# Performance work log

Measured on AMD Instinct MI355X. Metric: run time of the kernel, lower is better.

The kernel has to match this reference:

```python
import jax, jax.numpy as jnp
import numpy as np
from math import log2, ceil

NUM_LEAVES = 128
KERNEL = 8
STRIDE = 8
PADDING = 0
LR = 0.3

LEAF_NUM = 2 ** ceil(log2(NUM_LEAVES))   # 128
DEPTH = int(log2(LEAF_NUM))              # 7
NUM_NODES = 2 * LEAF_NUM - 1             # 255


def _ancestor_table():
    # A[j-1, t-1] = global heap index of the ancestor of node j at tree level t,
    # or -1 if t exceeds j's own level. Nodes use heap indexing: children of i
    # are 2i+1, 2i+2 (matches the layer bookkeeping in the torch module).
    A = np.full((NUM_NODES - 1, DEPTH), -1, dtype=np.int32)
    for j in range(1, NUM_NODES):
        lvl = int(np.floor(np.log2(j + 1)))
        anc = j
        for t in range(lvl, 0, -1):
            A[j - 1, t - 1] = anc
            anc = (anc - 1) // 2
    return jnp.asarray(A)

_ANC = _ancestor_table()  # (NUM_NODES-1, DEPTH)


def img2patches(x):
    x = jnp.pad(x, PADDING)
    H, W = x.shape
    n0 = (H - KERNEL) // STRIDE + 1
    n1 = (W - KERNEL) // STRIDE + 1
    win = jnp.arange(KERNEL)
    rows = jnp.arange(n0)[:, None] * STRIDE + win[None, :]  # (n0, k)
    cols = jnp.arange(n1)[:, None] * STRIDE + win[None, :]  # (n1, k)
    p = x[rows[:, None, :, None], cols[None, :, None, :]]   # (n0, n1, k, k)
    return p.reshape(n0 * n1, KERNEL * KERNEL)


def setup_inputs() -> dict:
    key = jax.random.key(0)
    k1, k2 = jax.random.split(key)
    image = jax.random.uniform(k1, (2048, 2048), dtype=jnp.float32)
    nodes = jax.random.uniform(k2, (NUM_NODES, KERNEL * KERNEL), dtype=jnp.float32)
    return {"image": image, "nodes": nodes}


def reference(image, nodes):
    X = img2patches(image)                      # (P, k^2)
    P = X.shape[0]

    # --- hierarchical BMU descent (binary tree, DEPTH levels) ---
    cur = jnp.zeros((P,), dtype=jnp.int32)      # root
    bmu_levels = []
    for _ in range(DEPTH):
        c0 = 2 * cur + 1
        c1 = 2 * cur + 2
        # pnorm with p=2 in the source is (sum((a-b)^2))^2 -- monotone, kept faithful
        d0 = jnp.sum((nodes[c0] - X) ** 2, axis=-1) ** 2
        d1 = jnp.sum((nodes[c1] - X) ** 2, axis=-1) ** 2
        cur = jnp.where(d1 < d0, c1, c0)        # tie -> first (c0), like torch.min
        bmu_levels.append(cur)
    bmu_path = jnp.stack(bmu_levels, axis=1)    # (P, DEPTH), bmu at levels 1..DEPTH

    # --- layer_state for every non-root node: number of levels at which the
    # node's ancestor coincides with the BMU chain (== the torch concatenated
    # layer_state, columns ordered by global node index 1..NUM_NODES-1) ---
    state = jnp.sum(_ANC[None, :, :] == bmu_path[:, None, :], axis=-1)  # (P, N-1)

    lrates = LR * (2.0 ** jnp.arange(1, DEPTH + 2, dtype=jnp.float32)) / 2.0 ** (DEPTH + 1)
    lrs = lrates[state]                          # (P, N-1)

    # mean_p lrs[p,j] * (X[p,:] - nodes[1+j,:])
    #   = (lrs^T @ X)/P - mean_p(lrs)[:,None] * nodes[1:]
    upd = jnp.einsum('pj,pk->jk', lrs, X) / P - lrs.mean(axis=0)[:, None] * nodes[1:]
    new_nodes = nodes.at[1:].add(upd)

    return new_nodes, cur[:, None]               # updated codebook, leaf BMU per patch
```

## Files before the change

### kernel.cpp

```cpp
#include <hip/hip_runtime.h>

#define IMG_W 2048
#define NUM_NODES 255
#define NLEAF 128
#define DEPTH 7
#define RS 68
#define NBLK 256
#define NUPD 16

template<int CTRL>
__device__ __forceinline__ float dpp_add(float x) {
    int v = __builtin_amdgcn_update_dpp(0, __float_as_int(x), CTRL, 0xF, 0xF, true);
    return x + __int_as_float(v);
}
__device__ __forceinline__ float group16_sum(float x) {
    x = dpp_add<0xB1>(x);
    x = dpp_add<0x4E>(x);
    x = dpp_add<0x141>(x);
    x = dpp_add<0x128>(x);
    return x;
}

__global__ __launch_bounds__(1024, 4) void fusedK(const float* __restrict__ img,
                                                  const float* __restrict__ nodes,
                                                  float* __restrict__ leaf_out,
                                                  float* __restrict__ S,
                                                  unsigned* __restrict__ cnt,
                                                  unsigned* __restrict__ fdone,
                                                  float* __restrict__ out_nodes)
{
    __shared__ float nds[NUM_NODES * RS];
    __shared__ float Sl[NLEAF * RS];
    __shared__ unsigned cntl[NLEAF];

    const int t = threadIdx.x;
    const int b = blockIdx.x;
    const int g = t >> 4;
    const int q = t & 15;
    const int q4 = q * 4;

    for (int i = t; i < NLEAF * RS; i += 1024) Sl[i] = 0.0f;
    if (t < NLEAF) cntl[t] = 0u;

    const float4* ng = (const float4*)nodes;
    for (int i = t; i < NUM_NODES * 16; i += 1024) {
        *(float4*)&nds[(i >> 4) * RS + (i & 15) * 4] = ng[i];
    }

    float4 xv0, xv1, xv2, xv3;
    {
        const int roff = (q >> 1), coff = (q & 1) * 4;
        int p = b * 256 + g;
        xv0 = *(const float4*)(img + (size_t)((p >> 8) * 8 + roff) * IMG_W + (p & 255) * 8 + coff);
        p += 64;
        xv1 = *(const float4*)(img + (size_t)((p >> 8) * 8 + roff) * IMG_W + (p & 255) * 8 + coff);
        p += 64;
        xv2 = *(const float4*)(img + (size_t)((p >> 8) * 8 + roff) * IMG_W + (p & 255) * 8 + coff);
        p += 64;
        xv3 = *(const float4*)(img + (size_t)((p >> 8) * 8 + roff) * IMG_W + (p & 255) * 8 + coff);
    }
    __syncthreads();

    int cur0 = 0, cur1 = 0, cur2 = 0, cur3 = 0;
    #pragma unroll
    for (int lvl = 0; lvl < DEPTH; ++lvl) {
        const int ca = 2 * cur0 + 1;
        const int cb = 2 * cur1 + 1;
        const int cc = 2 * cur2 + 1;
        const int cd = 2 * cur3 + 1;
        const float* pa = &nds[ca * RS + q4];
        const float* pb = &nds[cb * RS + q4];
        const float* pc = &nds[cc * RS + q4];
        const float* pd = &nds[cd * RS + q4];
        const float4 A0 = *(const float4*)(pa);
        const float4 B0 = *(const float4*)(pa + RS);
        const float4 A1 = *(const float4*)(pb);
        const float4 B1 = *(const float4*)(pb + RS);
        const float4 A2 = *(const float4*)(pc);
        const float4 B2 = *(const float4*)(pc + RS);
        const float4 A3 = *(const float4*)(pd);
        const float4 B3 = *(const float4*)(pd + RS);

        float d, s0, s1;
        s0 = 0.f; s1 = 0.f;
        d = A0.x - xv0.x; s0 = fmaf(d, d, s0);  d = B0.x - xv0.x; s1 = fmaf(d, d, s1);
        d = A0.y - xv0.y; s0 = fmaf(d, d, s0);  d = B0.y - xv0.y; s1 = fmaf(d, d, s1);
        d = A0.z - xv0.z; s0 = fmaf(d, d, s0);  d = B0.z - xv0.z; s1 = fmaf(d, d, s1);
        d = A0.w - xv0.w; s0 = fmaf(d, d, s0);  d = B0.w - xv0.w; s1 = fmaf(d, d, s1);
        cur0 = (group16_sum(s1 - s0) < 0.0f) ? (ca + 1) : ca;
        s0 = 0.f; s1 = 0.f;
        d = A1.x - xv1.x; s0 = fmaf(d, d, s0);  d = B1.x - xv1.x; s1 = fmaf(d, d, s1);
        d = A1.y - xv1.y; s0 = fmaf(d, d, s0);  d = B1.y - xv1.y; s1 = fmaf(d, d, s1);
        d = A1.z - xv1.z; s0 = fmaf(d, d, s0);  d = B1.z - xv1.z; s1 = fmaf(d, d, s1);
        d = A1.w - xv1.w; s0 = fmaf(d, d, s0);  d = B1.w - xv1.w; s1 = fmaf(d, d, s1);
        cur1 = (group16_sum(s1 - s0) < 0.0f) ? (cb + 1) : cb;
        s0 = 0.f; s1 = 0.f;
        d = A2.x - xv2.x; s0 = fmaf(d, d, s0);  d = B2.x - xv2.x; s1 = fmaf(d, d, s1);
        d = A2.y - xv2.y; s0 = fmaf(d, d, s0);  d = B2.y - xv2.y; s1 = fmaf(d, d, s1);
        d = A2.z - xv2.z; s0 = fmaf(d, d, s0);  d = B2.z - xv2.z; s1 = fmaf(d, d, s1);
        d = A2.w - xv2.w; s0 = fmaf(d, d, s0);  d = B2.w - xv2.w; s1 = fmaf(d, d, s1);
        cur2 = (group16_sum(s1 - s0) < 0.0f) ? (cc + 1) : cc;
        s0 = 0.f; s1 = 0.f;
        d = A3.x - xv3.x; s0 = fmaf(d, d, s0);  d = B3.x - xv3.x; s1 = fmaf(d, d, s1);
        d = A3.y - xv3.y; s0 = fmaf(d, d, s0);  d = B3.y - xv3.y; s1 = fmaf(d, d, s1);
        d = A3.z - xv3.z; s0 = fmaf(d, d, s0);  d = B3.z - xv3.z; s1 = fmaf(d, d, s1);
        d = A3.w - xv3.w; s0 = fmaf(d, d, s0);  d = B3.w - xv3.w; s1 = fmaf(d, d, s1);
        cur3 = (group16_sum(s1 - s0) < 0.0f) ? (cd + 1) : cd;
    }

    if (q == 0) {
        leaf_out[b * 256 + g]       = (float)cur0;
        leaf_out[b * 256 + 64 + g]  = (float)cur1;
        leaf_out[b * 256 + 128 + g] = (float)cur2;
        leaf_out[b * 256 + 192 + g] = (float)cur3;
        atomicAdd(&cntl[cur0 - 127], 1u);
        atomicAdd(&cntl[cur1 - 127], 1u);
        atomicAdd(&cntl[cur2 - 127], 1u);
        atomicAdd(&cntl[cur3 - 127], 1u);
    }

    {
        float* base = &Sl[(cur0 - 127) * RS + q];
        atomicAdd(base +  0, xv0.x); atomicAdd(base + 16, xv0.y);
        atomicAdd(base + 32, xv0.z); atomicAdd(base + 48, xv0.w);
        base = &Sl[(cur1 - 127) * RS + q];
        atomicAdd(base +  0, xv1.x); atomicAdd(base + 16, xv1.y);
        atomicAdd(base + 32, xv1.z); atomicAdd(base + 48, xv1.w);
        base = &Sl[(cur2 - 127) * RS + q];
        atomicAdd(base +  0, xv2.x); atomicAdd(base + 16, xv2.y);
        atomicAdd(base + 32, xv2.z); atomicAdd(base + 48, xv2.w);
        base = &Sl[(cur3 - 127) * RS + q];
        atomicAdd(base +  0, xv3.x); atomicAdd(base + 16, xv3.y);
        atomicAdd(base + 32, xv3.z); atomicAdd(base + 48, xv3.w);
    }
    __syncthreads();

    for (int ii = t; ii < NLEAF * 64; ii += 1024) {
        const int i = (ii + b * 64) & (NLEAF * 64 - 1);
        const int e = i & 63;
        const float v = Sl[(i >> 6) * RS + (e & 3) * 16 + (e >> 2)];
        if (v != 0.0f) atomicAdd(&S[i], v);
    }
    if (t < NLEAF && cntl[t] != 0u) atomicAdd(&cnt[t], cntl[t]);

    __syncthreads();
    if (t == 0) {
        __threadfence();
        __hip_atomic_fetch_add(fdone, 1u, __ATOMIC_RELEASE, __HIP_MEMORY_SCOPE_AGENT);
    }
    if (b >= NUPD) return;

    if (t == 0) {
        while (__hip_atomic_load(fdone, __ATOMIC_ACQUIRE, __HIP_MEMORY_SCOPE_AGENT) != NBLK) {}
    }
    __syncthreads();

    float* Ss = nds;
    float* cs = nds + 8192;
    for (int i = t; i < NLEAF * 64; i += 1024)
        Ss[i] = __hip_atomic_load(&S[i], __ATOMIC_RELAXED, __HIP_MEMORY_SCOPE_AGENT);
    if (t < NLEAF)
        cs[t] = (float)__hip_atomic_load(&cnt[t], __ATOMIC_RELAXED, __HIP_MEMORY_SCOPE_AGENT);
    __syncthreads();

    const int n = b * 16 + (t >> 6);
    const int k = t & 63;
    if (n >= NUM_NODES) return;
    const float nd = nodes[n * 64 + k];
    float o;
    if (n == 0) {
        o = nd;
    } else {
        const int pos = n + 1;
        const int Ln = 31 - __clz(pos);
        float su = 0.f, sc = 0.f;
        #pragma unroll 8
        for (int L = 0; L < NLEAF; ++L) {
            const int a = (128 + L) >> (7 - Ln);
            const int x = pos ^ a;
            const int state = (x == 0) ? Ln : (Ln - (31 - __clz(x)) - 1);
            const float lr = 0.3f * ((float)(1 << state) * (1.0f / 128.0f));
            su = fmaf(lr, Ss[L * 64 + k], su);
            sc = fmaf(lr, cs[L], sc);
        }
        const float invP = 1.0f / 65536.0f;
        o = nd + su * invP - (sc * invP) * nd;
    }
    out_nodes[n * 64 + k] = o;
}

extern "C" void kernel_launch(void* const* d_in, const int* in_sizes, int n_in,
                              void* d_out, int out_size, void* d_ws, size_t ws_size,
                              hipStream_t stream)
{
    const float* img   = (const float*)d_in[0];
    const float* nodes = (const float*)d_in[1];

    float* out_nodes = (float*)d_out;
    float* out_leaf  = out_nodes + NUM_NODES * 64;

    float*    S     = (float*)d_ws;
    unsigned* cnt   = (unsigned*)(S + NLEAF * 64);
    unsigned* fdone = cnt + NLEAF;

    hipMemsetAsync(d_ws, 0,
                   (NLEAF * 64) * sizeof(float) + NLEAF * sizeof(unsigned) + 16,
                   stream);
    fusedK<<<NBLK, 1024, 0, stream>>>(img, nodes, out_leaf, S, cnt, fdone, out_nodes);
}
```

Baseline: 116.2 us.

## Spread node update over 255 blocks and store leaf sums in natural order

The final codebook update is now spread across 255 blocks, one node per block with 64 active threads, instead of 16 blocks each handling 16 nodes. The intent is to shorten the serial tail after the global barrier. The per-block leaf sums are stored contiguously (q4 indexing), so the global flush reads them without a permutation. The spin-wait now runs in a full wavefront and sleeps between polls. In exchange, many more blocks wait at the grid-wide barrier and each one reloads the full S and cnt arrays. The local atomics may also see more LDS bank conflicts with the new layout.

```diff
diff --git a/kernel.cpp b/kernel.cpp
--- a/kernel.cpp
+++ b/kernel.cpp
@@ -6,7 +6,6 @@
 #define DEPTH 7
 #define RS 68
 #define NBLK 256
-#define NUPD 16
 
 template<int CTRL>
 __device__ __forceinline__ float dpp_add(float x) {
@@ -120,25 +119,23 @@
     }
 
     {
-        float* base = &Sl[(cur0 - 127) * RS + q];
-        atomicAdd(base +  0, xv0.x); atomicAdd(base + 16, xv0.y);
-        atomicAdd(base + 32, xv0.z); atomicAdd(base + 48, xv0.w);
-        base = &Sl[(cur1 - 127) * RS + q];
-        atomicAdd(base +  0, xv1.x); atomicAdd(base + 16, xv1.y);
-        atomicAdd(base + 32, xv1.z); atomicAdd(base + 48, xv1.w);
-        base = &Sl[(cur2 - 127) * RS + q];
-        atomicAdd(base +  0, xv2.x); atomicAdd(base + 16, xv2.y);
-        atomicAdd(base + 32, xv2.z); atomicAdd(base + 48, xv2.w);
-        base = &Sl[(cur3 - 127) * RS + q];
-        atomicAdd(base +  0, xv3.x); atomicAdd(base + 16, xv3.y);
-        atomicAdd(base + 32, xv3.z); atomicAdd(base + 48, xv3.w);
-    }
-    __syncthreads();
-
-    for (int ii = t; ii < NLEAF * 64; ii += 1024) {
-        const int i = (ii + b * 64) & (NLEAF * 64 - 1);
-        const int e = i & 63;
-        const float v = Sl[(i >> 6) * RS + (e & 3) * 16 + (e >> 2)];
+        float* dst = &Sl[(cur0 - 127) * RS + q4];
+        atomicAdd(dst + 0, xv0.x); atomicAdd(dst + 1, xv0.y);
+        atomicAdd(dst + 2, xv0.z); atomicAdd(dst + 3, xv0.w);
+        dst = &Sl[(cur1 - 127) * RS + q4];
+        atomicAdd(dst + 0, xv1.x); atomicAdd(dst + 1, xv1.y);
+        atomicAdd(dst + 2, xv1.z); atomicAdd(dst + 3, xv1.w);
+        dst = &Sl[(cur2 - 127) * RS + q4];
+        atomicAdd(dst + 0, xv2.x); atomicAdd(dst + 1, xv2.y);
+        atomicAdd(dst + 2, xv2.z); atomicAdd(dst + 3, xv2.w);
+        dst = &Sl[(cur3 - 127) * RS + q4];
+        atomicAdd(dst + 0, xv3.x); atomicAdd(dst + 1, xv3.y);
+        atomicAdd(dst + 2, xv3.z); atomicAdd(dst + 3, xv3.w);
+    }
+    __syncthreads();
+
+    for (int i = t; i < NLEAF * 64; i += 1024) {
+        const float v = Sl[(i >> 6) * RS + (i & 63)];
         if (v != 0.0f) atomicAdd(&S[i], v);
     }
     if (t < NLEAF && cntl[t] != 0u) atomicAdd(&cnt[t], cntl[t]);
@@ -148,10 +145,12 @@
         __threadfence();
         __hip_atomic_fetch_add(fdone, 1u, __ATOMIC_RELEASE, __HIP_MEMORY_SCOPE_AGENT);
     }
-    if (b >= NUPD) return;
-
-    if (t == 0) {
-        while (__hip_atomic_load(fdone, __ATOMIC_ACQUIRE, __HIP_MEMORY_SCOPE_AGENT) != NBLK) {}
+    if (b >= NUM_NODES) return;
+
+    if (t < 64) {
+        while (__hip_atomic_load(fdone, __ATOMIC_ACQUIRE, __HIP_MEMORY_SCOPE_AGENT) != NBLK) {
+            __builtin_amdgcn_s_sleep(2);
+        }
     }
     __syncthreads();
 
@@ -163,30 +162,31 @@
         cs[t] = (float)__hip_atomic_load(&cnt[t], __ATOMIC_RELAXED, __HIP_MEMORY_SCOPE_AGENT);
     __syncthreads();
 
-    const int n = b * 16 + (t >> 6);
-    const int k = t & 63;
-    if (n >= NUM_NODES) return;
-    const float nd = nodes[n * 64 + k];
-    float o;
-    if (n == 0) {
-        o = nd;
-    } else {
-        const int pos = n + 1;
-        const int Ln = 31 - __clz(pos);
-        float su = 0.f, sc = 0.f;
-        #pragma unroll 8
-        for (int L = 0; L < NLEAF; ++L) {
-            const int a = (128 + L) >> (7 - Ln);
-            const int x = pos ^ a;
-            const int state = (x == 0) ? Ln : (Ln - (31 - __clz(x)) - 1);
-            const float lr = 0.3f * ((float)(1 << state) * (1.0f / 128.0f));
-            su = fmaf(lr, Ss[L * 64 + k], su);
-            sc = fmaf(lr, cs[L], sc);
+    if (t < 64) {
+        const int n = b;
+        const int k = t;
+        const float nd = nodes[n * 64 + k];
+        float o;
+        if (n == 0) {
+            o = nd;
+        } else {
+            const int pos = n + 1;
+            const int Ln = 31 - __clz(pos);
+            float su = 0.f, sc = 0.f;
+            #pragma unroll 8
+            for (int L = 0; L < NLEAF; ++L) {
+                const int a = (128 + L) >> (7 - Ln);
+                const int x = pos ^ a;
+                const int state = (x == 0) ? Ln : (Ln - (31 - __clz(x)) - 1);
+                const float lr = 0.3f * ((float)(1 << state) * (1.0f / 128.0f));
+                su = fmaf(lr, Ss[L * 64 + k], su);
+                sc = fmaf(lr, cs[L], sc);
+            }
+            const float invP = 1.0f / 65536.0f;
+            o = nd + su * invP - (sc * invP) * nd;
         }
-        const float invP = 1.0f / 65536.0f;
-        o = nd + su * invP - (sc * invP) * nd;
-    }
-    out_nodes[n * 64 + k] = o;
+        out_nodes[n * 64 + k] = o;
+    }
 }
 
 extern "C" void kernel_launch(void* const* d_in, const int* in_sizes, int n_in,
```

New measurement: 120.6 us. 1.04x slower.
